# Kernel optimization log

Measured on AMD Instinct MI355X. Metric: run time of the kernel, lower is better.

The kernel has to match this reference:

```python
import jax, jax.numpy as jnp
import numpy as np

N, K, D = 131072, 1024, 128
COMMITMENT_COST = 0.25


def setup_inputs() -> dict:
    key = jax.random.key(0)
    k1, k2 = jax.random.split(key)
    c_input = jax.random.normal(k1, (N, D), dtype=jnp.float32)
    # nn.Embedding weight initialized N(0, 0.1)
    embedding_weight = jax.random.normal(k2, (K, D), dtype=jnp.float32) * 0.1
    return {"c_input": c_input, "embedding_weight": embedding_weight}


def reference(c_input, embedding_weight):
    distances = (
        jnp.sum(c_input ** 2, axis=1, keepdims=True)
        + jnp.sum(embedding_weight ** 2, axis=1)
        - 2.0 * jnp.matmul(c_input, embedding_weight.T)
    )
    encoding_indices = jnp.argmin(distances, axis=1)  # [N]
    encodings = jax.nn.one_hot(encoding_indices, K, dtype=c_input.dtype)  # [N, K]
    # one-hot @ weight == direct gather
    quantized = embedding_weight[encoding_indices]  # [N, D]
    e_latent_loss = jnp.mean((jax.lax.stop_gradient(quantized) - c_input) ** 2)
    q_latent_loss = jnp.mean((quantized - jax.lax.stop_gradient(c_input)) ** 2)
    loss = q_latent_loss + COMMITMENT_COST * e_latent_loss
    # straight-through estimator
    quantized_st = c_input + jax.lax.stop_gradient(quantized - c_input)
    return (loss, quantized_st, encodings)
```

## Files before the change

kernel.cpp:

```cpp
#include <hip/hip_runtime.h>
#include <hip/hip_bf16.h>

#define NROWS 131072
#define KC 1024
#define DD 128
#define MARGIN 1e-3f

typedef __attribute__((ext_vector_type(8))) short short8;
typedef __attribute__((ext_vector_type(4))) float f32x4;

__device__ inline short f2bf_hi(float f) {
  unsigned u = __builtin_bit_cast(unsigned, f);
  u += 0x7fffu + ((u >> 16) & 1u);
  return (short)(u >> 16);
}
__device__ inline float bf2f(short s) {
  unsigned u = ((unsigned)(unsigned short)s) << 16;
  return __builtin_bit_cast(float, u);
}

__global__ void vq_prep(const float* __restrict__ E, short* __restrict__ EH,
                        short* __restrict__ EL, float* __restrict__ SE,
                        float* __restrict__ out) {
  int b = blockIdx.x, t = threadIdx.x;
  if (b < 64) {
    int idx = b * 256 + t;
    int s = (idx >> 6) & 3, l = idx & 63;
    int c = idx >> 8;
    int q = l >> 4, n = l & 15;
    const float* src = E + (16 * c + n) * DD + 32 * s + 8 * q;
    short8 h, lo;
#pragma unroll
    for (int j = 0; j < 8; ++j) {
      float x = src[j];
      short hb = f2bf_hi(x);
      h[j] = hb;
      lo[j] = f2bf_hi(x - bf2f(hb));
    }
    *(short8*)(EH + idx * 8) = h;
    *(short8*)(EL + idx * 8) = lo;
  } else {
    if (t == 0) out[0] = 0.f;
    for (int k = t; k < KC; k += 256) {
      double acc = 0.0;
      const float* er = E + k * DD;
      for (int i = 0; i < DD; ++i) { double v = (double)er[i]; acc += v * v; }
      SE[k] = (float)acc;
    }
  }
}

__global__ __launch_bounds__(256, 3) void vq_argmin(
    const float* __restrict__ X, const float* __restrict__ E,
    const short* __restrict__ EH, const short* __restrict__ EL,
    const float* __restrict__ SE, int* __restrict__ IDX) {
  __shared__ __align__(16) short lbh[8192];
  __shared__ __align__(16) short lbl[8192];
  __shared__ int lidx[128];
  __shared__ int lflag[128];
  __shared__ int lany;
  __shared__ float lx[128];
  __shared__ float lrv[256];
  __shared__ int lri[256];
  __shared__ float lsx;

  const int tid = threadIdx.x;
  const int w = tid >> 6, l = tid & 63, q = l >> 4, n = l & 15;
  const int row_base = blockIdx.x * 128;
  if (tid == 0) lany = 0;

  short8 ah[2][4], al[2][4];
#pragma unroll
  for (int mt = 0; mt < 2; ++mt) {
    const float* xp = X + (row_base + 32 * w + 16 * mt + n) * DD + 8 * q;
#pragma unroll
    for (int s = 0; s < 4; ++s) {
      f32x4 x0 = *(const f32x4*)(xp + 32 * s);
      f32x4 x1 = *(const f32x4*)(xp + 32 * s + 4);
#pragma unroll
      for (int j = 0; j < 4; ++j) {
        short hb = f2bf_hi(x0[j]);
        ah[mt][s][j] = hb;
        al[mt][s][j] = f2bf_hi(x0[j] - bf2f(hb));
        short hb2 = f2bf_hi(x1[j]);
        ah[mt][s][j + 4] = hb2;
        al[mt][s][j + 4] = f2bf_hi(x1[j] - bf2f(hb2));
      }
    }
  }

  float bestv[8], secv[8];
  int besti[8];
#pragma unroll
  for (int i = 0; i < 8; ++i) { bestv[i] = -3e38f; secv[i] = -3e38f; besti[i] = 0; }

  for (int cc = 0; cc < 16; ++cc) {
    {
      const short8* gh = (const short8*)(EH + cc * 8192);
      const short8* gl = (const short8*)(EL + cc * 8192);
      short8* dh = (short8*)lbh;
      short8* dl = (short8*)lbl;
#pragma unroll
      for (int i = 0; i < 4; ++i) {
        int u = i * 256 + tid;
        dh[u] = gh[u];
        dl[u] = gl[u];
      }
    }
    __syncthreads();

    f32x4 acc[2][4];
#pragma unroll
    for (int mt = 0; mt < 2; ++mt)
#pragma unroll
      for (int nt = 0; nt < 4; ++nt) acc[mt][nt] = (f32x4){0.f, 0.f, 0.f, 0.f};

#pragma unroll
    for (int nt = 0; nt < 4; ++nt) {
#pragma unroll
      for (int s = 0; s < 4; ++s) {
        short8 bh  = *(const short8*)(lbh + ((nt * 4 + s) * 64 + l) * 8);
        short8 blo = *(const short8*)(lbl + ((nt * 4 + s) * 64 + l) * 8);
        acc[0][nt] = __builtin_amdgcn_mfma_f32_16x16x32_bf16(ah[0][s], bh,  acc[0][nt], 0, 0, 0);
        acc[1][nt] = __builtin_amdgcn_mfma_f32_16x16x32_bf16(ah[1][s], bh,  acc[1][nt], 0, 0, 0);
        acc[0][nt] = __builtin_amdgcn_mfma_f32_16x16x32_bf16(al[0][s], bh,  acc[0][nt], 0, 0, 0);
        acc[1][nt] = __builtin_amdgcn_mfma_f32_16x16x32_bf16(al[1][s], bh,  acc[1][nt], 0, 0, 0);
        acc[0][nt] = __builtin_amdgcn_mfma_f32_16x16x32_bf16(ah[0][s], blo, acc[0][nt], 0, 0, 0);
        acc[1][nt] = __builtin_amdgcn_mfma_f32_16x16x32_bf16(ah[1][s], blo, acc[1][nt], 0, 0, 0);
      }
    }
    __syncthreads();

#pragma unroll
    for (int nt = 0; nt < 4; ++nt) {
      int k = cc * 64 + nt * 16 + n;
      float hse = 0.5f * SE[k];
#pragma unroll
      for (int mt = 0; mt < 2; ++mt)
#pragma unroll
        for (int r = 0; r < 4; ++r) {
          float sc = acc[mt][nt][r] - hse;
          int slot = mt * 4 + r;
          bool gt = sc > bestv[slot];
          secv[slot] = gt ? bestv[slot] : fmaxf(secv[slot], sc);
          if (gt) { bestv[slot] = sc; besti[slot] = k; }
        }
    }
  }

#pragma unroll
  for (int slot = 0; slot < 8; ++slot) {
    float v = bestv[slot], s2 = secv[slot];
    int bi = besti[slot];
#pragma unroll
    for (int m = 1; m <= 8; m <<= 1) {
      float v2 = __shfl_xor(v, m, 64);
      float sv2 = __shfl_xor(s2, m, 64);
      int i2 = __shfl_xor(bi, m, 64);
      float ns = fmaxf(fminf(v, v2), fmaxf(s2, sv2));
      if (v2 > v || (v2 == v && i2 < bi)) { v = v2; bi = i2; }
      s2 = ns;
    }
    if (n == 0) {
      int mt = slot >> 2, r = slot & 3;
      int rl = 32 * w + 16 * mt + 4 * q + r;
      int f = (v - s2) <= MARGIN;
      lidx[rl] = bi;
      lflag[rl] = f;
      if (f) lany = 1;
    }
  }
  __syncthreads();

  if (lany) {
    for (int rl = 0; rl < 128; ++rl) {
      if (lflag[rl] == 0) continue;
      if (tid < DD) lx[tid] = X[(row_base + rl) * DD + tid];
      __syncthreads();
      if (tid == 0) {
        double sx = 0.0;
        for (int i = 0; i < DD; ++i) { double v = (double)lx[i]; sx += v * v; }
        lsx = (float)sx;
      }
      __syncthreads();
      float dmin = 3e38f; int kmin = 0;
      for (int kk = tid; kk < KC; kk += 256) {
        double dot = 0.0;
        const float* er = E + kk * DD;
        for (int i = 0; i < DD; ++i) dot += (double)lx[i] * (double)er[i];
        float a = lsx + SE[kk];
        float b2 = (float)(2.0 * dot);
        float dnp = a - b2;
        if (dnp < dmin) { dmin = dnp; kmin = kk; }
      }
      lrv[tid] = dmin; lri[tid] = kmin;
      __syncthreads();
      if (tid == 0) {
        float dm = lrv[0]; int km = lri[0];
        for (int t2 = 1; t2 < 256; ++t2)
          if (lrv[t2] < dm || (lrv[t2] == dm && lri[t2] < km)) { dm = lrv[t2]; km = lri[t2]; }
        lidx[rl] = km;
      }
      __syncthreads();
    }
  }
  __syncthreads();

  if (tid < 128) IDX[row_base + tid] = lidx[tid];
}

__global__ __launch_bounds__(256) void vq_out(
    const float* __restrict__ X, const float* __restrict__ E,
    const int* __restrict__ IDX, float* __restrict__ out) {
  __shared__ float lloss[4];
  const int tid = threadIdx.x;
  const int w = tid >> 6, l = tid & 63;
  const int row0 = blockIdx.x * 64 + w * 16;
  const int encb = 1 + NROWS * DD;

  float lp = 0.f;
  for (int i = 0; i < 16; ++i) {
    int row = row0 + i;
    int idx = IDX[row];
    float x0 = X[row * DD + l];
    float x1 = X[row * DD + 64 + l];
    float e0 = E[idx * DD + l];
    float e1 = E[idx * DD + 64 + l];
    float d0 = e0 - x0, d1 = e1 - x1;
    __builtin_nontemporal_store(x0 + d0, out + 1 + row * DD + l);
    __builtin_nontemporal_store(x1 + d1, out + 1 + row * DD + 64 + l);
    lp += d0 * d0 + d1 * d1;
    float* ob = out + encb + row * KC;
    if (l < 3) __builtin_nontemporal_store((l == idx) ? 1.f : 0.f, ob + l);
    for (int c = l; c < 255; c += 64) {
      int eb = 3 + 4 * c;
      f32x4 v;
      v[0] = (eb     == idx) ? 1.f : 0.f;
      v[1] = (eb + 1 == idx) ? 1.f : 0.f;
      v[2] = (eb + 2 == idx) ? 1.f : 0.f;
      v[3] = (eb + 3 == idx) ? 1.f : 0.f;
      __builtin_nontemporal_store(v, (f32x4*)(ob + eb));
    }
    if (l == 63) __builtin_nontemporal_store((1023 == idx) ? 1.f : 0.f, ob + 1023);
  }
#pragma unroll
  for (int m = 1; m < 64; m <<= 1) lp += __shfl_xor(lp, m, 64);
  if (l == 0) lloss[w] = lp;
  __syncthreads();
  if (tid == 0) {
    float t = (lloss[0] + lloss[1] + lloss[2] + lloss[3]) *
              (1.25f / ((float)NROWS * (float)DD));
    atomicAdd(out, t);
  }
}

extern "C" void kernel_launch(void* const* d_in, const int* in_sizes, int n_in,
                              void* d_out, int out_size, void* d_ws, size_t ws_size,
                              hipStream_t stream) {
  const float* X = (const float*)d_in[0];
  const float* E = (const float*)d_in[1];
  float* out = (float*)d_out;
  short* EH = (short*)d_ws;
  short* EL = EH + KC * DD;
  float* SE = (float*)(EL + KC * DD);
  int* IDX = (int*)(SE + KC);
  vq_prep<<<65, 256, 0, stream>>>(E, EH, EL, SE, out);
  vq_argmin<<<NROWS / 128, 256, 0, stream>>>(X, E, EH, EL, SE, IDX);
  vq_out<<<NROWS / 64, 256, 0, stream>>>(X, E, IDX, out);
}
```

Measured before the change: 925.9 us.

## Fuse output kernel into argmin kernel and memset the one-hot encodings

Merges the separate output kernel into the argmin kernel, so quantized outputs and loss come straight from indices held in shared memory and the index buffer round trip goes away. The dense one-hot write is replaced by a hipMemsetAsync that zeroes the encodings, followed by a single scattered store of 1.0 per row. Launch bounds are raised to four blocks per SM. The large zero fill still runs as its own memset pass, and the higher occupancy target may cause register spills.

Result: no change. 908.7 us (-1.9%).

```diff
diff --git a/kernel.cpp b/kernel.cpp
--- a/kernel.cpp
+++ b/kernel.cpp
@@ -50,10 +50,10 @@
   }
 }
 
-__global__ __launch_bounds__(256, 3) void vq_argmin(
+__global__ __launch_bounds__(256, 4) void vq_main(
     const float* __restrict__ X, const float* __restrict__ E,
     const short* __restrict__ EH, const short* __restrict__ EL,
-    const float* __restrict__ SE, int* __restrict__ IDX) {
+    const float* __restrict__ SE, float* __restrict__ out) {
   __shared__ __align__(16) short lbh[8192];
   __shared__ __align__(16) short lbl[8192];
   __shared__ int lidx[128];
@@ -63,6 +63,7 @@
   __shared__ float lrv[256];
   __shared__ int lri[256];
   __shared__ float lsx;
+  __shared__ float lloss[4];
 
   const int tid = threadIdx.x;
   const int w = tid >> 6, l = tid & 63, q = l >> 4, n = l & 15;
@@ -206,22 +207,11 @@
   }
   __syncthreads();
 
-  if (tid < 128) IDX[row_base + tid] = lidx[tid];
-}
-
-__global__ __launch_bounds__(256) void vq_out(
-    const float* __restrict__ X, const float* __restrict__ E,
-    const int* __restrict__ IDX, float* __restrict__ out) {
-  __shared__ float lloss[4];
-  const int tid = threadIdx.x;
-  const int w = tid >> 6, l = tid & 63;
-  const int row0 = blockIdx.x * 64 + w * 16;
+  float lp = 0.f;
   const int encb = 1 + NROWS * DD;
-
-  float lp = 0.f;
-  for (int i = 0; i < 16; ++i) {
-    int row = row0 + i;
-    int idx = IDX[row];
+  for (int rl = w; rl < 128; rl += 4) {
+    int row = row_base + rl;
+    int idx = lidx[rl];
     float x0 = X[row * DD + l];
     float x1 = X[row * DD + 64 + l];
     float e0 = E[idx * DD + l];
@@ -230,18 +220,7 @@
     __builtin_nontemporal_store(x0 + d0, out + 1 + row * DD + l);
     __builtin_nontemporal_store(x1 + d1, out + 1 + row * DD + 64 + l);
     lp += d0 * d0 + d1 * d1;
-    float* ob = out + encb + row * KC;
-    if (l < 3) __builtin_nontemporal_store((l == idx) ? 1.f : 0.f, ob + l);
-    for (int c = l; c < 255; c += 64) {
-      int eb = 3 + 4 * c;
-      f32x4 v;
-      v[0] = (eb     == idx) ? 1.f : 0.f;
-      v[1] = (eb + 1 == idx) ? 1.f : 0.f;
-      v[2] = (eb + 2 == idx) ? 1.f : 0.f;
-      v[3] = (eb + 3 == idx) ? 1.f : 0.f;
-      __builtin_nontemporal_store(v, (f32x4*)(ob + eb));
-    }
-    if (l == 63) __builtin_nontemporal_store((1023 == idx) ? 1.f : 0.f, ob + 1023);
+    if (l == 0) out[encb + row * KC + idx] = 1.0f;
   }
 #pragma unroll
   for (int m = 1; m < 64; m <<= 1) lp += __shfl_xor(lp, m, 64);
@@ -263,8 +242,8 @@
   short* EH = (short*)d_ws;
   short* EL = EH + KC * DD;
   float* SE = (float*)(EL + KC * DD);
-  int* IDX = (int*)(SE + KC);
+  size_t encb = (size_t)1 + (size_t)NROWS * DD;
+  hipMemsetAsync(out + encb, 0, (size_t)NROWS * KC * sizeof(float), stream);
   vq_prep<<<65, 256, 0, stream>>>(E, EH, EL, SE, out);
-  vq_argmin<<<NROWS / 128, 256, 0, stream>>>(X, E, EH, EL, SE, IDX);
-  vq_out<<<NROWS / 64, 256, 0, stream>>>(X, E, IDX, out);
-}
+  vq_main<<<NROWS / 128, 256, 0, stream>>>(X, E, EH, EL, SE, out);
+}
```
